# Optimization experiments

Measured on AMD Instinct MI355X. Metric: run time of the kernel, lower is better.

## Reference

```python
import jax, jax.numpy as jnp
import numpy as np

T, B, NHID = 64, 32, 768
NB, BS = 6, 128          # num_blocks, block_size = nhid // num_blocks
TOPK = 4                 # active blocks per step
NTOK = 32000
ATT = 4 * BS             # input-attention value dim (att_out), per RIMs BlocksCore
DK = 64                  # input-attention key dim
NH2, DK2 = 4, 16         # communication attention heads / head dim


def setup_inputs() -> dict:
    key = jax.random.key(0)
    ks = jax.random.split(key, 16)
    s = 0.02
    return {
        "x": jax.random.normal(ks[0], (T, B, NHID), jnp.float32),
        "hx0": jax.random.normal(ks[1], (B, NHID), jnp.float32),
        "cx0": jax.random.normal(ks[2], (B, NHID), jnp.float32),
        # input attention (1 head): per-read-block query proj, per-write-slot key/value proj
        "Wq_in": jax.random.normal(ks[3], (NB, BS, DK), jnp.float32) * s,
        "Wk_in": jax.random.normal(ks[4], (2, NHID, DK), jnp.float32) * s,
        "Wv_in": jax.random.normal(ks[5], (2, NHID, ATT), jnp.float32) * s,
        # block-diagonal LSTM (blockify_params): per-block weights
        "Wih": jax.random.normal(ks[6], (NB, ATT, 4 * BS), jnp.float32) * s,
        "Whh": jax.random.normal(ks[7], (NB, BS, 4 * BS), jnp.float32) * s,
        "b_lstm": jnp.zeros((NB, 4 * BS), jnp.float32),
        # communication attention (4 heads, dk=dv=16), per-block projections + output proj
        "Wq_c": jax.random.normal(ks[8], (NB, BS, NH2 * DK2), jnp.float32) * s,
        "Wk_c": jax.random.normal(ks[9], (NB, BS, NH2 * DK2), jnp.float32) * s,
        "Wv_c": jax.random.normal(ks[10], (NB, BS, NH2 * DK2), jnp.float32) * s,
        "Wo_c": jax.random.normal(ks[11], (NB, NH2 * DK2, BS), jnp.float32) * s,
        # decoder
        "Wd": jax.random.normal(ks[12], (NTOK, NHID), jnp.float32) * 0.1,
        "bd": jnp.zeros((NTOK,), jnp.float32),
    }


def _step(hx, cx, xt, Wq_in, Wk_in, Wv_in, Wih, Whh, b_lstm, Wq_c, Wk_c, Wv_c, Wo_c):
    hb = hx.reshape(B, NB, BS)
    cb = cx.reshape(B, NB, BS)
    # --- input attention: each block reads from {null, input} slots ---
    kv_in = jnp.stack([jnp.zeros_like(xt), xt], axis=1)          # [B,2,NHID]
    q = jnp.einsum('bnd,ndk->bnk', hb, Wq_in)                    # [B,NB,DK]
    k = jnp.einsum('bmd,mdk->bmk', kv_in, Wk_in)                 # [B,2,DK]
    v = jnp.einsum('bmd,mdv->bmv', kv_in, Wv_in)                 # [B,2,ATT]
    iatt = jax.nn.softmax(
        jnp.einsum('bnk,bmk->bnm', q, k) / jnp.sqrt(jnp.float32(DK)), axis=-1)
    inp_use = jnp.einsum('bnm,bmv->bnv', iatt, v)                # [B,NB,ATT]
    # --- top-k block routing: drop NB-TOPK blocks attending most to null ---
    null_att = iatt[:, :, 0]                                     # [B,NB]
    _, drop_idx = jax.lax.top_k(null_att, NB - TOPK)
    mask = jnp.ones((B, NB), hx.dtype).at[
        jnp.arange(B)[:, None], drop_idx].set(0.0)               # [B,NB]
    # --- per-block (block-diagonal) LSTM ---
    gates = (jnp.einsum('bnv,nvg->bng', inp_use, Wih)
             + jnp.einsum('bnh,nhg->bng', hb, Whh) + b_lstm)     # [B,NB,4*BS]
    i, f, g, o = jnp.split(gates, 4, axis=-1)
    c_new = jax.nn.sigmoid(f) * cb + jax.nn.sigmoid(i) * jnp.tanh(g)
    h_new = jax.nn.sigmoid(o) * jnp.tanh(c_new)                  # [B,NB,BS]
    # --- communication attention among blocks (residual) ---
    q2 = jnp.einsum('bnd,ndk->bnk', h_new, Wq_c).reshape(B, NB, NH2, DK2)
    k2 = jnp.einsum('bnd,ndk->bnk', h_new, Wk_c).reshape(B, NB, NH2, DK2)
    v2 = jnp.einsum('bnd,ndk->bnk', h_new, Wv_c).reshape(B, NB, NH2, DK2)
    att = jax.nn.softmax(
        jnp.einsum('bihk,bjhk->bhij', q2, k2) / jnp.sqrt(jnp.float32(DK2)), axis=-1)
    comm = jnp.einsum('bhij,bjhv->bihv', att, v2).reshape(B, NB, NH2 * DK2)
    h_new = h_new + jnp.einsum('bnk,nkd->bnd', comm, Wo_c)
    # --- gated state update: inactive blocks keep old state ---
    m = mask[:, :, None]
    hx_next = (m * h_new + (1.0 - m) * hb).reshape(B, NHID)
    cx_next = (m * c_new + (1.0 - m) * cb).reshape(B, NHID)
    return hx_next, cx_next


def reference(x, hx0, cx0, Wq_in, Wk_in, Wv_in, Wih, Whh, b_lstm,
              Wq_c, Wk_c, Wv_c, Wo_c, Wd, bd):
    def scan_step(carry, xt):
        hx, cx = carry
        hx, cx = _step(hx, cx, xt, Wq_in, Wk_in, Wv_in, Wih, Whh, b_lstm,
                       Wq_c, Wk_c, Wv_c, Wo_c)
        return (hx, cx), hx
    (hx, cx), outs = jax.lax.scan(scan_step, (hx0, cx0), x)     # outs: [T,B,NHID]
    decoded = outs.reshape(T * B, NHID) @ Wd.T + bd              # [T*B,NTOK]
    return decoded, hx, cx
```

## Files before the change

### kernel.cpp

```cpp
#include <hip/hip_runtime.h>
#include <hip/hip_bf16.h>
#include <stdint.h>

#define TT 64
#define BB 32
#define NHIDC 768
#define NBK 6
#define BSZ 128
#define NTOKC 32000

using f32x4  = __attribute__((ext_vector_type(4))) float;
using f32x2  = __attribute__((ext_vector_type(2))) float;
using short8 = __attribute__((ext_vector_type(8))) short;

#define OFF_FLG   0u
#define OFF_XPUB  4096u
#define OFF_HTB   8065024u
#define OFF_K1    11210752u
#define OFF_V1    11735040u
#define OFF_U     15929344u
#define OFF_WDB   41095168u

__device__ __forceinline__ float sigf(float x){ return 1.f/(1.f + expf(-x)); }

__device__ __forceinline__ void stc(float* p, float v){
  __hip_atomic_store(p, v, __ATOMIC_RELAXED, __HIP_MEMORY_SCOPE_AGENT);
}
__device__ __forceinline__ float ldc(const float* p){
  return __hip_atomic_load(p, __ATOMIC_RELAXED, __HIP_MEMORY_SCOPE_AGENT);
}
#define VMCNT0 asm volatile("s_waitcnt vmcnt(0)" ::: "memory")
#define CBAR   asm volatile("" ::: "memory")

__device__ __forceinline__ void gload16(const void* g, void* l){
  __builtin_amdgcn_global_load_lds(
      (const __attribute__((address_space(1))) unsigned int*)g,
      (__attribute__((address_space(3))) unsigned int*)l, 16, 0, 0);
}

__device__ __forceinline__ int xslot(int par, int gg, int nn, int b){
  return (((par*16 + gg)*6 + nn)*2 + b)*132;
}

__global__ void prep_kernel(const float* __restrict__ Wd,
                            unsigned short* __restrict__ Wdb,
                            unsigned int* __restrict__ flags)
{
  if (blockIdx.x == 0 && threadIdx.x < 128)
    __hip_atomic_store(flags + threadIdx.x, 0u, __ATOMIC_RELAXED, __HIP_MEMORY_SCOPE_AGENT);
  int i = blockIdx.x*blockDim.x + threadIdx.x;
  const int n = NTOKC*NHIDC;
  const int stride = gridDim.x*blockDim.x;
  for (; i < n; i += stride){
    __hip_bfloat16 h = __float2bfloat16(Wd[i]);
    Wdb[i] = *reinterpret_cast<unsigned short*>(&h);
  }
}

template<int TM, int TN>
__global__ __launch_bounds__(256) void gemm_f32(
    const float* __restrict__ A, int lda,
    const float* __restrict__ B, int ldb, long bstride,
    float* __restrict__ C, int ldc, long cstride,
    int N, int K)
{
  constexpr int BM = 16*TM, BN = 16*TN;
  __shared__ float As[16][BM];
  __shared__ float Bs[16][BN+4];
  const float* Bb = B + (long)blockIdx.z * bstride;
  float* Cb = C + (long)blockIdx.z * cstride;
  const int m0 = blockIdx.x*BM, n0 = blockIdx.y*BN;
  const int tid = threadIdx.x, tx = tid & 15, ty = tid >> 4;
  float acc[TM][TN];
  #pragma unroll
  for (int i=0;i<TM;++i)
    #pragma unroll
    for (int j=0;j<TN;++j) acc[i][j]=0.f;

  for (int k0=0; k0<K; k0+=16){
    if constexpr (TM == 8){
      const int r = tid>>1, kk = (tid&1)*8;
      const float4 v0 = *(const float4*)&A[(long)(m0+r)*lda + k0 + kk];
      const float4 v1 = *(const float4*)&A[(long)(m0+r)*lda + k0 + kk + 4];
      As[kk+0][r]=v0.x; As[kk+1][r]=v0.y; As[kk+2][r]=v0.z; As[kk+3][r]=v0.w;
      As[kk+4][r]=v1.x; As[kk+5][r]=v1.y; As[kk+6][r]=v1.z; As[kk+7][r]=v1.w;
    } else {
      const int r = tid>>2, kk = (tid&3)*4;
      const float4 v0 = *(const float4*)&A[(long)(m0+r)*lda + k0 + kk];
      As[kk+0][r]=v0.x; As[kk+1][r]=v0.y; As[kk+2][r]=v0.z; As[kk+3][r]=v0.w;
    }
    if constexpr (TN == 8){
      const int rb = tid>>4, cb = (tid&15)*8;
      float4 v0 = {0,0,0,0}, v1 = {0,0,0,0};
      if (n0+cb+4 <= N) v0 = *(const float4*)&Bb[(long)(k0+rb)*ldb + n0+cb];
      if (n0+cb+8 <= N) v1 = *(const float4*)&Bb[(long)(k0+rb)*ldb + n0+cb+4];
      *(float4*)&Bs[rb][cb]   = v0;
      *(float4*)&Bs[rb][cb+4] = v1;
    } else {
      const int rb = tid>>4, cb = (tid&15)*4;
      float4 v0 = {0,0,0,0};
      if (n0+cb+4 <= N) v0 = *(const float4*)&Bb[(long)(k0+rb)*ldb + n0+cb];
      *(float4*)&Bs[rb][cb] = v0;
    }
    __syncthreads();
    #pragma unroll
    for (int kk=0; kk<16; ++kk){
      float av[TM], bv[TN];
      #pragma unroll
      for (int i=0;i<TM;++i) av[i] = As[kk][ty*TM+i];
      #pragma unroll
      for (int j=0;j<TN;++j) bv[j] = Bs[kk][tx*TN+j];
      #pragma unroll
      for (int i=0;i<TM;++i)
        #pragma unroll
        for (int j=0;j<TN;++j) acc[i][j] += av[i]*bv[j];
    }
    __syncthreads();
  }
  #pragma unroll
  for (int i=0;i<TM;++i){
    const int row = m0 + ty*TM + i;
    #pragma unroll
    for (int j=0;j<TN;++j){
      const int col = n0 + tx*TN + j;
      if (col < N) Cb[(long)row*ldc + col] = acc[i][j];
    }
  }
}

__global__ __launch_bounds__(1024, 2) void recurrent_kernel(
    const float* __restrict__ hx0, const float* __restrict__ cx0,
    const float* __restrict__ Wq_in, const float* __restrict__ Whh,
    const float* __restrict__ b_lstm,
    const float* __restrict__ Wk_c, const float* __restrict__ Wv_c,
    const float* __restrict__ Wq_c, const float* __restrict__ Wo_c,
    const float* __restrict__ K1buf, const float* __restrict__ Ubuf,
    float* __restrict__ xpub, unsigned int* __restrict__ flags,
    unsigned short* __restrict__ HTx,
    float* __restrict__ out_hx, float* __restrict__ out_cx)
{
  const int w = blockIdx.x, gg = w/6, n = w - gg*6, tid = threadIdx.x;

  __shared__ float WcT[192*130];
  __shared__ float WqL[128*65];
  __shared__ float hL[2][128], cL[2][128], h0L[2][128], cnL[2][128];
  __shared__ float gatesL[2][512];
  __shared__ float partL[2][2][512];
  __shared__ float kvqL[2][192];
  __shared__ float kvAll[2][6][130];
  __shared__ float attL[2][4][6], attW[2][4][6];
  __shared__ float commL[2][64];
  __shared__ float nullAll[2][6], sL[2], nullLoc[2], maskL[2];

  const int kh = tid >> 9, gc = tid & 511;
  const int od = tid >> 3, okq = tid & 7;

  f32x4 whr[16];
  {
    const float* src = Whh + (long)n*65536 + kh*64*512 + gc;
    #pragma unroll
    for (int r4=0; r4<16; ++r4){
      f32x4 v;
      v[0] = src[(r4*4+0)*512]; v[1] = src[(r4*4+1)*512];
      v[2] = src[(r4*4+2)*512]; v[3] = src[(r4*4+3)*512];
      whr[r4] = v;
    }
  }
  #pragma unroll
  for (int i=0;i<16;++i) asm volatile("" : "+v"(whr[i]));
  f32x4 wo0, wo1;
  {
    const float* src = Wo_c + n*8192 + od;
    #pragma unroll
    for (int j=0;j<4;++j) wo0[j] = src[(okq*8+j)*128];
    #pragma unroll
    for (int j=0;j<4;++j) wo1[j] = src[(okq*8+4+j)*128];
  }
  asm volatile("" : "+v"(wo0));
  asm volatile("" : "+v"(wo1));
  const float blr = b_lstm[n*512 + gc];

  for (int i = tid; i < 8192; i += 1024){
    const int h = i>>6, c = i&63;
    WcT[(c    )*130 + h] = Wk_c[n*8192 + i];
    WcT[(c+ 64)*130 + h] = Wv_c[n*8192 + i];
    WcT[(c+128)*130 + h] = Wq_c[n*8192 + i];
    WqL[h*65 + c] = Wq_in[n*8192 + i];
  }
  if (tid < 256){
    const int b = tid>>7, d = tid&127;
    hL[b][d] = hx0[(gg*2+b)*768 + n*128 + d];
    cL[b][d] = cx0[(gg*2+b)*768 + n*128 + d];
  }
  __syncthreads();

  for (int t = 0; t < TT; ++t){
    const int par = t & 1;
    float u0 = 0.f, u1 = 0.f, k1r = 0.f;
    if (kh == 0){
      u0 = Ubuf[((long)(t*32 + gg*2+0)*6 + n)*512 + gc];
      u1 = Ubuf[((long)(t*32 + gg*2+1)*6 + n)*512 + gc];
    }
    if (tid < 128) k1r = K1buf[(long)(t*32 + gg*2 + (tid>>6))*64 + (tid&63)];

    {
      float gd0 = 0.f, gd1 = 0.f;
      #pragma unroll
      for (int r4 = 0; r4 < 16; ++r4){
        const f32x4 h0v = *(const f32x4*)&hL[0][kh*64 + r4*4];
        const f32x4 h1v = *(const f32x4*)&hL[1][kh*64 + r4*4];
        #pragma unroll
        for (int j=0;j<4;++j){
          gd0 += whr[r4][j]*h0v[j];
          gd1 += whr[r4][j]*h1v[j];
        }
      }
      partL[0][kh][gc] = gd0;
      partL[1][kh][gc] = gd1;
    }
    if (tid < 128){
      const int b = tid>>6, k = tid&63;
      float q = 0.f;
      #pragma unroll 16
      for (int h=0; h<128; ++h) q += WqL[h*65 + k]*hL[b][h];
      float term = q*k1r;
      #pragma unroll
      for (int off=32; off; off>>=1) term += __shfl_xor(term, off);
      if (k == 0){
        const float l1 = term*0.125f;
        const float mx = fmaxf(l1, 0.f);
        const float e0 = expf(0.f-mx), e1 = expf(l1-mx);
        const float inv = 1.f/(e0+e1);
        sL[b] = e1*inv; nullLoc[b] = e0*inv;
      }
    }
    __syncthreads();
    if (kh == 0){
      gatesL[0][gc] = partL[0][0][gc] + partL[0][1][gc] + sL[0]*u0 + blr;
      gatesL[1][gc] = partL[1][0][gc] + partL[1][1][gc] + sL[1]*u1 + blr;
    }
    __syncthreads();
    if (tid < 256){
      const int b = tid>>7, dd = tid&127;
      const float gi = gatesL[b][dd],     gf = gatesL[b][128+dd];
      const float gG = gatesL[b][256+dd], go = gatesL[b][384+dd];
      const float cp = cL[b][dd];
      const float cn = sigf(gf)*cp + sigf(gi)*tanhf(gG);
      const float h0 = sigf(go)*tanhf(cn);
      cnL[b][dd] = cn; h0L[b][dd] = h0;
    }
    __syncthreads();
    if (tid < 384){
      const int b = tid/192, c = tid%192;
      float a = 0.f;
      #pragma unroll
      for (int h4=0; h4<32; ++h4){
        const f32x2 wa = *(const f32x2*)&WcT[c*130 + h4*4];
        const f32x2 wb = *(const f32x2*)&WcT[c*130 + h4*4 + 2];
        const f32x4 hv = *(const f32x4*)&h0L[b][h4*4];
        a += wa[0]*hv[0] + wa[1]*hv[1] + wb[0]*hv[2] + wb[1]*hv[3];
      }
      kvqL[b][c] = a;
    }
    __syncthreads();
    if (tid < 256){
      const int b = tid>>7, idx = tid&127;
      stc(&xpub[xslot(par,gg,n,b) + idx], kvqL[b][idx]);
    }
    if (tid < 2) stc(&xpub[xslot(par,gg,n,tid) + 128], nullLoc[tid]);
    VMCNT0;
    __syncthreads();
    if (tid < 6){
      if (tid == 0)
        __hip_atomic_store(&flags[gg*8+n], (unsigned)(t+1), __ATOMIC_RELAXED, __HIP_MEMORY_SCOPE_AGENT);
      while (__hip_atomic_load(&flags[gg*8+tid], __ATOMIC_RELAXED, __HIP_MEMORY_SCOPE_AGENT) < (unsigned)(t+1))
        __builtin_amdgcn_s_sleep(1);
    }
    __syncthreads(); CBAR;
    for (int idx = tid; idx < 1536; idx += 1024){
      const int j = idx/256, r = idx&255, b = r>>7, c = r&127;
      kvAll[b][j][c] = ldc(&xpub[xslot(par,gg,j,b) + c]);
    }
    if (tid < 12){
      const int j = tid>>1, b = tid&1;
      nullAll[b][j] = ldc(&xpub[xslot(par,gg,j,b) + 128]);
    }
    __syncthreads();
    if (tid < 48){
      const int b = tid/24, h = (tid/6)%4, j = tid%6;
      float lg = 0.f;
      #pragma unroll
      for (int kk=0; kk<16; ++kk)
        lg += kvqL[b][128 + h*16 + kk]*kvAll[b][j][h*16 + kk];
      attL[b][h][j] = lg*0.25f;
    }
    if (tid >= 48 && tid < 50){
      const int b = tid - 48;
      const float own = nullAll[b][n];
      int rank = 0;
      #pragma unroll
      for (int j=0;j<6;++j){
        const float v = nullAll[b][j];
        rank += (v > own || (v == own && j < n)) ? 1 : 0;
      }
      maskL[b] = (rank < 2) ? 0.f : 1.f;
    }
    __syncthreads();
    if (tid < 8){
      const int b = tid>>2, h = tid&3;
      float mx = attL[b][h][0];
      #pragma unroll
      for (int j=1;j<6;++j) mx = fmaxf(mx, attL[b][h][j]);
      float e[6], sum = 0.f;
      #pragma unroll
      for (int j=0;j<6;++j){ e[j] = expf(attL[b][h][j]-mx); sum += e[j]; }
      const float inv = 1.f/sum;
      #pragma unroll
      for (int j=0;j<6;++j) attW[b][h][j] = e[j]*inv;
    }
    __syncthreads();
    if (tid < 128){
      const int b = tid>>6, hv = tid&63, h = hv>>4, v = hv&15;
      float s2 = 0.f;
      #pragma unroll
      for (int j=0;j<6;++j) s2 += attW[b][h][j]*kvAll[b][j][64 + h*16 + v];
      commL[b][hv] = s2;
    }
    __syncthreads();
    {
      #pragma unroll
      for (int b=0; b<2; ++b){
        float a = 0.f;
        #pragma unroll
        for (int j=0;j<4;++j) a += commL[b][okq*8+j]*wo0[j];
        #pragma unroll
        for (int j=0;j<4;++j) a += commL[b][okq*8+4+j]*wo1[j];
        a += __shfl_xor(a,1); a += __shfl_xor(a,2); a += __shfl_xor(a,4);
        if (okq == 0 && maskL[b] != 0.f){
          hL[b][od] = h0L[b][od] + a;
          cL[b][od] = cnL[b][od];
        }
      }
    }
    __syncthreads();
    if (tid < 256){
      const int b = tid>>7, d = tid&127;
      const float hv = hL[b][d];
      __hip_bfloat16 hb16 = __float2bfloat16(hv);
      HTx[(long)(t*32 + gg*2 + b)*768 + n*128 + d] = *reinterpret_cast<unsigned short*>(&hb16);
      if (t == TT-1){
        out_hx[(gg*2+b)*768 + n*128 + d] = hv;
        out_cx[(gg*2+b)*768 + n*128 + d] = cL[b][d];
      }
    }
  }
}

__global__ __launch_bounds__(256) void decoder_kernel(
    const unsigned short* __restrict__ A,
    const unsigned short* __restrict__ Bw,
    const float* __restrict__ bd,
    float* __restrict__ out)
{
  __shared__ unsigned short As[4096];
  __shared__ unsigned short Bs[4096];
  const int m0 = blockIdx.x*128, n0 = blockIdx.y*128;
  const int tid = threadIdx.x;
  const int wv = tid >> 6, lane = tid & 63;
  const int wm = wv >> 1, wn = wv & 1;
  const int r16 = lane & 15, krow = lane >> 4;

  f32x4 acc[4][4] = {};

  for (int k0 = 0; k0 < 768; k0 += 32){
    #pragma unroll
    for (int i=0; i<2; ++i){
      const int idx = i*256 + tid;
      const int row = idx >> 2, k8 = (idx & 3)*8;
      gload16(&A [(long)(m0+row)*768 + k0 + k8], (char*)As + i*4096 + wv*1024);
      gload16(&Bw[(long)(n0+row)*768 + k0 + k8], (char*)Bs + i*4096 + wv*1024);
    }
    __syncthreads();
    short8 af[4], bf[4];
    #pragma unroll
    for (int mi=0; mi<4; ++mi)
      af[mi] = *(const short8*)&As[(wm*64 + mi*16 + r16)*32 + krow*8];
    #pragma unroll
    for (int ni=0; ni<4; ++ni)
      bf[ni] = *(const short8*)&Bs[(wn*64 + ni*16 + r16)*32 + krow*8];
    #pragma unroll
    for (int mi=0; mi<4; ++mi)
      #pragma unroll
      for (int ni=0; ni<4; ++ni)
        acc[mi][ni] = __builtin_amdgcn_mfma_f32_16x16x32_bf16(af[mi], bf[ni], acc[mi][ni], 0, 0, 0);
    __syncthreads();
  }

  #pragma unroll
  for (int ni=0; ni<4; ++ni){
    const int col = n0 + wn*64 + ni*16 + r16;
    const float bv = bd[col];
    #pragma unroll
    for (int mi=0; mi<4; ++mi){
      const int rbase = m0 + wm*64 + mi*16 + krow*4;
      #pragma unroll
      for (int j=0; j<4; ++j)
        out[(size_t)(rbase + j)*NTOKC + col] = acc[mi][ni][j] + bv;
    }
  }
}

extern "C" void kernel_launch(void* const* d_in, const int* in_sizes, int n_in,
                              void* d_out, int out_size, void* d_ws, size_t ws_size,
                              hipStream_t stream)
{
  (void)in_sizes; (void)n_in; (void)out_size; (void)ws_size;
  const float* x      = (const float*)d_in[0];
  const float* hx0    = (const float*)d_in[1];
  const float* cx0    = (const float*)d_in[2];
  const float* Wq_in  = (const float*)d_in[3];
  const float* Wk_in  = (const float*)d_in[4];
  const float* Wv_in  = (const float*)d_in[5];
  const float* Wih    = (const float*)d_in[6];
  const float* Whh    = (const float*)d_in[7];
  const float* b_lstm = (const float*)d_in[8];
  const float* Wq_c   = (const float*)d_in[9];
  const float* Wk_c   = (const float*)d_in[10];
  const float* Wv_c   = (const float*)d_in[11];
  const float* Wo_c   = (const float*)d_in[12];
  const float* Wd     = (const float*)d_in[13];
  const float* bd     = (const float*)d_in[14];

  char* ws = (char*)d_ws;
  unsigned int*  flg  = (unsigned int*)(ws + OFF_FLG);
  float*         xpub = (float*)(ws + OFF_XPUB);
  unsigned short* HTx = (unsigned short*)(ws + OFF_HTB);
  float*         K1b  = (float*)(ws + OFF_K1);
  float*         V1b  = (float*)(ws + OFF_V1);
  float*         Ub   = (float*)(ws + OFF_U);
  unsigned short* Wdb = (unsigned short*)(ws + OFF_WDB);

  float* out_dec = (float*)d_out;
  float* out_hx  = out_dec + (size_t)2048*NTOKC;
  float* out_cx  = out_hx + BB*NHIDC;

  prep_kernel<<<2048, 256, 0, stream>>>(Wd, Wdb, flg);
  gemm_f32<4,4><<<dim3(32,1,1), 256, 0, stream>>>(x, NHIDC, Wk_in + 768*64, 64, 0,
                                                  K1b, 64, 0, 64, NHIDC);
  gemm_f32<4,4><<<dim3(32,8,1), 256, 0, stream>>>(x, NHIDC, Wv_in + 768*512, 512, 0,
                                                  V1b, 512, 0, 512, NHIDC);
  gemm_f32<8,8><<<dim3(16,4,6), 256, 0, stream>>>(V1b, 512, Wih, 512, (long)512*512,
                                                  Ub, 3072, 512, 512, 512);
  recurrent_kernel<<<96, 1024, 0, stream>>>(hx0, cx0, Wq_in, Whh, b_lstm,
                                            Wk_c, Wv_c, Wq_c, Wo_c,
                                            K1b, Ub, xpub, flg, HTx,
                                            out_hx, out_cx);
  decoder_kernel<<<dim3(16,250,1), 256, 0, stream>>>(HTx, Wdb, bd, out_dec);
}
```

Measured before the change: 1.259 ms.

## Cut barriers in recurrent step, vectorize Wd conversion, remap decoder tiles

The recurrent kernel now folds gate assembly into the LSTM cell stage and publishes the null score directly from the attention step. It also writes kv values to the exchange buffer straight from registers, and merges the communication logits, softmax, weighted sum and top-k mask into one 64-thread wave using shuffles. Together these remove several __syncthreads per timestep on the serial critical path. Separately, the bf16 weight conversion uses float4 loads, and the decoder uses a 1D grid with a swizzled tile mapping so that concurrent blocks are spread across the 8 XCDs. The risk is extra LDS traffic for the bias and U values, and the tile mapping is tied to the 4000-block grid size.

```diff
diff --git a/kernel.cpp b/kernel.cpp
--- a/kernel.cpp
+++ b/kernel.cpp
@@ -49,11 +49,16 @@
   if (blockIdx.x == 0 && threadIdx.x < 128)
     __hip_atomic_store(flags + threadIdx.x, 0u, __ATOMIC_RELAXED, __HIP_MEMORY_SCOPE_AGENT);
   int i = blockIdx.x*blockDim.x + threadIdx.x;
-  const int n = NTOKC*NHIDC;
+  const int n4 = NTOKC*NHIDC/4;
   const int stride = gridDim.x*blockDim.x;
-  for (; i < n; i += stride){
-    __hip_bfloat16 h = __float2bfloat16(Wd[i]);
-    Wdb[i] = *reinterpret_cast<unsigned short*>(&h);
+  for (; i < n4; i += stride){
+    const float4 v = ((const float4*)Wd)[i];
+    ushort4 o;
+    __hip_bfloat16 b0 = __float2bfloat16(v.x); o.x = *reinterpret_cast<unsigned short*>(&b0);
+    __hip_bfloat16 b1 = __float2bfloat16(v.y); o.y = *reinterpret_cast<unsigned short*>(&b1);
+    __hip_bfloat16 b2 = __float2bfloat16(v.z); o.z = *reinterpret_cast<unsigned short*>(&b2);
+    __hip_bfloat16 b3 = __float2bfloat16(v.w); o.w = *reinterpret_cast<unsigned short*>(&b3);
+    ((ushort4*)Wdb)[i] = o;
   }
 }
 
@@ -144,13 +149,14 @@
   __shared__ float WcT[192*130];
   __shared__ float WqL[128*65];
   __shared__ float hL[2][128], cL[2][128], h0L[2][128], cnL[2][128];
-  __shared__ float gatesL[2][512];
   __shared__ float partL[2][2][512];
+  __shared__ float uL[2][512];
+  __shared__ float blL[512];
   __shared__ float kvqL[2][192];
   __shared__ float kvAll[2][6][130];
-  __shared__ float attL[2][4][6], attW[2][4][6];
   __shared__ float commL[2][64];
-  __shared__ float nullAll[2][6], sL[2], nullLoc[2], maskL[2];
+  __shared__ float nullAll[2][8];
+  __shared__ float sL[2], maskL[2];
 
   const int kh = tid >> 9, gc = tid & 511;
   const int od = tid >> 3, okq = tid & 7;
@@ -178,8 +184,8 @@
   }
   asm volatile("" : "+v"(wo0));
   asm volatile("" : "+v"(wo1));
-  const float blr = b_lstm[n*512 + gc];
-
+
+  if (tid < 512) blL[tid] = b_lstm[n*512 + tid];
   for (int i = tid; i < 8192; i += 1024){
     const int h = i>>6, c = i&63;
     WcT[(c    )*130 + h] = Wk_c[n*8192 + i];
@@ -196,11 +202,8 @@
 
   for (int t = 0; t < TT; ++t){
     const int par = t & 1;
-    float u0 = 0.f, u1 = 0.f, k1r = 0.f;
-    if (kh == 0){
-      u0 = Ubuf[((long)(t*32 + gg*2+0)*6 + n)*512 + gc];
-      u1 = Ubuf[((long)(t*32 + gg*2+1)*6 + n)*512 + gc];
-    }
+    uL[kh][gc] = Ubuf[((long)(t*32 + gg*2 + kh)*6 + n)*512 + gc];
+    float k1r = 0.f;
     if (tid < 128) k1r = K1buf[(long)(t*32 + gg*2 + (tid>>6))*64 + (tid&63)];
 
     {
@@ -231,19 +234,18 @@
         const float mx = fmaxf(l1, 0.f);
         const float e0 = expf(0.f-mx), e1 = expf(l1-mx);
         const float inv = 1.f/(e0+e1);
-        sL[b] = e1*inv; nullLoc[b] = e0*inv;
-      }
-    }
-    __syncthreads();
-    if (kh == 0){
-      gatesL[0][gc] = partL[0][0][gc] + partL[0][1][gc] + sL[0]*u0 + blr;
-      gatesL[1][gc] = partL[1][0][gc] + partL[1][1][gc] + sL[1]*u1 + blr;
+        sL[b] = e1*inv;
+        stc(&xpub[xslot(par,gg,n,b) + 128], e0*inv);
+      }
     }
     __syncthreads();
     if (tid < 256){
       const int b = tid>>7, dd = tid&127;
-      const float gi = gatesL[b][dd],     gf = gatesL[b][128+dd];
-      const float gG = gatesL[b][256+dd], go = gatesL[b][384+dd];
+      const float s = sL[b];
+      const float gi = partL[b][0][dd]     + partL[b][1][dd]     + s*uL[b][dd]     + blL[dd];
+      const float gf = partL[b][0][128+dd] + partL[b][1][128+dd] + s*uL[b][128+dd] + blL[128+dd];
+      const float gG = partL[b][0][256+dd] + partL[b][1][256+dd] + s*uL[b][256+dd] + blL[256+dd];
+      const float go = partL[b][0][384+dd] + partL[b][1][384+dd] + s*uL[b][384+dd] + blL[384+dd];
       const float cp = cL[b][dd];
       const float cn = sigf(gf)*cp + sigf(gi)*tanhf(gG);
       const float h0 = sigf(go)*tanhf(cn);
@@ -261,13 +263,8 @@
         a += wa[0]*hv[0] + wa[1]*hv[1] + wb[0]*hv[2] + wb[1]*hv[3];
       }
       kvqL[b][c] = a;
-    }
-    __syncthreads();
-    if (tid < 256){
-      const int b = tid>>7, idx = tid&127;
-      stc(&xpub[xslot(par,gg,n,b) + idx], kvqL[b][idx]);
-    }
-    if (tid < 2) stc(&xpub[xslot(par,gg,n,tid) + 128], nullLoc[tid]);
+      if (c < 128) stc(&xpub[xslot(par,gg,n,b) + c], a);
+    }
     VMCNT0;
     __syncthreads();
     if (tid < 6){
@@ -286,45 +283,45 @@
       nullAll[b][j] = ldc(&xpub[xslot(par,gg,j,b) + 128]);
     }
     __syncthreads();
-    if (tid < 48){
-      const int b = tid/24, h = (tid/6)%4, j = tid%6;
-      float lg = 0.f;
-      #pragma unroll
-      for (int kk=0; kk<16; ++kk)
-        lg += kvqL[b][128 + h*16 + kk]*kvAll[b][j][h*16 + kk];
-      attL[b][h][j] = lg*0.25f;
-    }
-    if (tid >= 48 && tid < 50){
-      const int b = tid - 48;
-      const float own = nullAll[b][n];
-      int rank = 0;
+    if (tid < 64){
+      const int lane = tid;
+      const int g5 = lane>>3, l3 = lane&7;
+      const int b = g5>>2, h = g5&3;
+      float lg = -1e30f;
+      if (l3 < 6){
+        float s = 0.f;
+        #pragma unroll
+        for (int kk=0; kk<16; ++kk)
+          s += kvqL[b][128 + h*16 + kk]*kvAll[b][l3][h*16 + kk];
+        lg = s*0.25f;
+      }
+      float mx = lg;
+      mx = fmaxf(mx, __shfl_xor(mx,1));
+      mx = fmaxf(mx, __shfl_xor(mx,2));
+      mx = fmaxf(mx, __shfl_xor(mx,4));
+      float ev = (l3 < 6) ? expf(lg - mx) : 0.f;
+      float sum = ev;
+      sum += __shfl_xor(sum,1); sum += __shfl_xor(sum,2); sum += __shfl_xor(sum,4);
+      const float myw = ev/sum;
+      float s0 = 0.f, s1 = 0.f;
       #pragma unroll
       for (int j=0;j<6;++j){
-        const float v = nullAll[b][j];
-        rank += (v > own || (v == own && j < n)) ? 1 : 0;
-      }
-      maskL[b] = (rank < 2) ? 0.f : 1.f;
-    }
-    __syncthreads();
-    if (tid < 8){
-      const int b = tid>>2, h = tid&3;
-      float mx = attL[b][h][0];
-      #pragma unroll
-      for (int j=1;j<6;++j) mx = fmaxf(mx, attL[b][h][j]);
-      float e[6], sum = 0.f;
-      #pragma unroll
-      for (int j=0;j<6;++j){ e[j] = expf(attL[b][h][j]-mx); sum += e[j]; }
-      const float inv = 1.f/sum;
-      #pragma unroll
-      for (int j=0;j<6;++j) attW[b][h][j] = e[j]*inv;
-    }
-    __syncthreads();
-    if (tid < 128){
-      const int b = tid>>6, hv = tid&63, h = hv>>4, v = hv&15;
-      float s2 = 0.f;
-      #pragma unroll
-      for (int j=0;j<6;++j) s2 += attW[b][h][j]*kvAll[b][j][64 + h*16 + v];
-      commL[b][hv] = s2;
+        const float wj = __shfl(myw, g5*8 + j);
+        s0 += wj*kvAll[b][j][64 + h*16 + l3*2];
+        s1 += wj*kvAll[b][j][64 + h*16 + l3*2 + 1];
+      }
+      commL[b][h*16 + l3*2]     = s0;
+      commL[b][h*16 + l3*2 + 1] = s1;
+      if (lane < 2){
+        const float own = nullAll[lane][n];
+        int rank = 0;
+        #pragma unroll
+        for (int j=0;j<6;++j){
+          const float v = nullAll[lane][j];
+          rank += (v > own || (v == own && j < n)) ? 1 : 0;
+        }
+        maskL[lane] = (rank < 2) ? 0.f : 1.f;
+      }
     }
     __syncthreads();
     {
@@ -364,7 +361,9 @@
 {
   __shared__ unsigned short As[4096];
   __shared__ unsigned short Bs[4096];
-  const int m0 = blockIdx.x*128, n0 = blockIdx.y*128;
+  const int bid = blockIdx.x;
+  const int tile = (bid & 7)*500 + (bid >> 3);
+  const int m0 = (tile & 15)*128, n0 = (tile >> 4)*128;
   const int tid = threadIdx.x;
   const int wv = tid >> 6, lane = tid & 63;
   const int wm = wv >> 1, wn = wv & 1;
@@ -455,5 +454,5 @@
                                             Wk_c, Wv_c, Wq_c, Wo_c,
                                             K1b, Ub, xpub, flg, HTx,
                                             out_hx, out_cx);
-  decoder_kernel<<<dim3(16,250,1), 256, 0, stream>>>(HTx, Wdb, bd, out_dec);
-}
+  decoder_kernel<<<4000, 256, 0, stream>>>(HTx, Wdb, bd, out_dec);
+}
```

Result: slower. 1.311 ms (+4.1%).
